# Kernel tuning notes

Hardware: AMD Instinct MI355X
Metric: run time of the kernel (lower is better)

## Reference

```python
import jax, jax.numpy as jnp
import numpy as np

B, F, V, E, T, NTOK, G, D = 8192, 64, 1000, 64, 2, 16, 4, 256
LN_EPS = 1e-5


def setup_inputs() -> dict:
    key = jax.random.key(0)
    ks = jax.random.split(key, 5)
    int_feats = jax.random.randint(ks[0], (B, F), 0, V, dtype=jnp.int64)
    missing_mask = jax.random.randint(ks[1], (B, F), 0, 2, dtype=jnp.int32)
    # deterministic seeded permutation of features split into NTOK equal groups
    perm = np.random.default_rng(1234).permutation(F)
    group_idx = jnp.asarray(perm.reshape(NTOK, G), dtype=jnp.int32)
    emb_tables = jax.random.normal(ks[2], (T, F, V, E), jnp.float32) * 0.02
    missing_emb = jax.random.normal(ks[3], (T, F, E), jnp.float32) * 0.02
    kW, kb = jax.random.split(ks[4])
    W = jax.random.normal(kW, (D, E * T), jnp.float32) * (1.0 / np.sqrt(E * T))
    b = jnp.zeros((D,), jnp.float32)
    ln_gamma = jnp.ones((D,), jnp.float32)
    ln_beta = jnp.zeros((D,), jnp.float32)
    return {"int_feats": int_feats, "missing_mask": missing_mask,
            "group_idx": group_idx, "emb_tables": emb_tables,
            "missing_emb": missing_emb, "W": W, "b": b,
            "ln_gamma": ln_gamma, "ln_beta": ln_beta}


def reference(int_feats, missing_mask, group_idx, emb_tables, missing_emb, W, b, ln_gamma, ln_beta):
    f_idx = jnp.arange(F)[None, :]  # (1, F) broadcast with (B, F) ids
    # per-table feature embedding gather: [T, B, F, E]
    feats = jax.vmap(lambda tbl: tbl[f_idx, int_feats])(emb_tables)
    # additive missing embeddings
    mask = missing_mask.astype(feats.dtype)
    feats = feats + mask[None, :, :, None] * missing_emb[:, None, :, :]
    # token-group mean pooling: [T, B, NTOK, G, E] -> [T, B, NTOK, E]
    pooled = feats[:, :, group_idx, :].mean(axis=3)
    # concat tables along feature dim (table order preserved): [B, NTOK, T*E]
    x = jnp.moveaxis(pooled, 0, 2).reshape(B, NTOK, T * E)
    # Linear -> SiLU -> LayerNorm
    h = jax.nn.silu(x @ W.T + b)
    mu = h.mean(-1, keepdims=True)
    var = ((h - mu) ** 2).mean(-1, keepdims=True)
    return (h - mu) * jax.lax.rsqrt(var + LN_EPS) * ln_gamma + ln_beta
```

## Files before the change

### kernel.cpp

```cpp
#include <hip/hip_runtime.h>
#include <math.h>

#define B_    8192
#define F_    64
#define V_    1000
#define E_    64
#define T_    2
#define NTOK_ 16
#define G_    4
#define D_    256
#define K_    128
#define LN_EPS 1e-5f

#define XSP   136

typedef __attribute__((ext_vector_type(8))) short  frag_ab;
typedef __attribute__((ext_vector_type(4))) float  frag_cd;

static __device__ __forceinline__ unsigned short f2bf(float f) {
    unsigned int u = __float_as_uint(f);
    u += 0x7FFFu + ((u >> 16) & 1u);
    return (unsigned short)(u >> 16);
}

__global__ __launch_bounds__(256) void convert_w_kernel(const float* __restrict__ W,
                                                        unsigned int* __restrict__ Wb_packed) {
    const int i = blockIdx.x * 256 + threadIdx.x;
    if (i < (D_ * K_) / 2) {
        const float2 v = *(const float2*)(W + (size_t)i * 2);
        Wb_packed[i] = (unsigned int)f2bf(v.x) | ((unsigned int)f2bf(v.y) << 16);
    }
}

__global__ __launch_bounds__(256, 8) void fused_tokenizer_kernel(
    const int*   __restrict__ int_feats,
    const int*   __restrict__ missing_mask,
    const int*   __restrict__ group_idx,
    const float* __restrict__ emb_tables,
    const float* __restrict__ missing_emb,
    const unsigned short* __restrict__ Wb,
    const float* __restrict__ bias,
    const float* __restrict__ gamma,
    const float* __restrict__ beta,
    float*       __restrict__ out)
{
    __shared__ unsigned short xs[NTOK_][XSP];
    __shared__ unsigned int   soff[F_];
    __shared__ int            smask[F_];
    __shared__ int            sg[F_];
    __shared__ float          part_s [4][NTOK_];
    __shared__ float          part_ss[4][NTOK_];

    const int tid  = threadIdx.x;
    const int b    = blockIdx.x;
    const int lane = tid & 63;
    const int wave = tid >> 6;
    const int mA   = lane & 15;
    const int q    = lane >> 4;

    if (tid < F_) {
        const int f  = tid;
        const int id = int_feats[b * F_ + f];
        soff[f]  = (unsigned int)((f * V_ + id) * E_);
        smask[f] = missing_mask[b * F_ + f];
        sg[f]    = group_idx[f];
    }
    __syncthreads();

#pragma unroll
    for (int i = 0; i < 2; ++i) {
        const int c  = i * 256 + tid;
        const int n  = c >> 5;
        const int r4 = c & 31;
        const int t  = r4 >> 4;
        const int e  = (r4 & 15) * 4;
        const float* bt = emb_tables + (size_t)t * (F_ * V_ * E_) + e;
        const float* mt = missing_emb + t * (F_ * E_) + e;
        float ax = 0.f, ay = 0.f, az = 0.f, aw = 0.f;
#pragma unroll
        for (int g = 0; g < G_; ++g) {
            const int f = sg[n * G_ + g];
            const float4 v = *(const float4*)(bt + soff[f]);
            float vx = v.x, vy = v.y, vz = v.z, vw = v.w;
            if (smask[f]) {
                const float4 mv = *(const float4*)(mt + f * E_);
                vx += mv.x; vy += mv.y; vz += mv.z; vw += mv.w;
            }
            ax += vx; ay += vy; az += vz; aw += vw;
        }
        unsigned int p0 = (unsigned int)f2bf(0.25f * ax) | ((unsigned int)f2bf(0.25f * ay) << 16);
        unsigned int p1 = (unsigned int)f2bf(0.25f * az) | ((unsigned int)f2bf(0.25f * aw) << 16);
        *(uint2*)(&xs[n][r4 * 4]) = make_uint2(p0, p1);
    }
    __syncthreads();

    frag_ab a[4];
#pragma unroll
    for (int s = 0; s < 4; ++s)
        a[s] = *(const frag_ab*)(&xs[mA][32 * s + 8 * q]);

    float hv[4][4];
    float ps[4]  = {0.f, 0.f, 0.f, 0.f};
    float pss[4] = {0.f, 0.f, 0.f, 0.f};

#pragma unroll
    for (int t = 0; t < 4; ++t) {
        const int nrow = wave * 64 + t * 16 + mA;
        const unsigned short* wp = Wb + (size_t)nrow * K_ + 8 * q;
        frag_cd acc = {0.f, 0.f, 0.f, 0.f};
#pragma unroll
        for (int s = 0; s < 4; ++s) {
            const frag_ab bfr = *(const frag_ab*)(wp + 32 * s);
            acc = __builtin_amdgcn_mfma_f32_16x16x32_bf16(a[s], bfr, acc, 0, 0, 0);
        }
        const float bn = bias[nrow];
#pragma unroll
        for (int reg = 0; reg < 4; ++reg) {
            const float z = acc[reg] + bn;
            const float h = z / (1.f + __expf(-z));
            hv[t][reg] = h;
            ps[reg]  += h;
            pss[reg] += h * h;
        }
    }

#pragma unroll
    for (int off = 1; off < 16; off <<= 1) {
#pragma unroll
        for (int reg = 0; reg < 4; ++reg) {
            ps[reg]  += __shfl_xor(ps[reg],  off, 64);
            pss[reg] += __shfl_xor(pss[reg], off, 64);
        }
    }
    if (mA == 0) {
        *(float4*)(&part_s [wave][q * 4]) = make_float4(ps[0],  ps[1],  ps[2],  ps[3]);
        *(float4*)(&part_ss[wave][q * 4]) = make_float4(pss[0], pss[1], pss[2], pss[3]);
    }
    __syncthreads();

    float4 S0 = *(const float4*)(&part_s [0][q * 4]);
    float4 S1 = *(const float4*)(&part_s [1][q * 4]);
    float4 S2 = *(const float4*)(&part_s [2][q * 4]);
    float4 S3 = *(const float4*)(&part_s [3][q * 4]);
    float4 T0 = *(const float4*)(&part_ss[0][q * 4]);
    float4 T1 = *(const float4*)(&part_ss[1][q * 4]);
    float4 T2 = *(const float4*)(&part_ss[2][q * 4]);
    float4 T3 = *(const float4*)(&part_ss[3][q * 4]);

    float mu[4], rs[4];
    {
        const float s[4]  = {S0.x + S1.x + S2.x + S3.x, S0.y + S1.y + S2.y + S3.y,
                             S0.z + S1.z + S2.z + S3.z, S0.w + S1.w + S2.w + S3.w};
        const float ss[4] = {T0.x + T1.x + T2.x + T3.x, T0.y + T1.y + T2.y + T3.y,
                             T0.z + T1.z + T2.z + T3.z, T0.w + T1.w + T2.w + T3.w};
#pragma unroll
        for (int reg = 0; reg < 4; ++reg) {
            mu[reg] = s[reg] * (1.f / D_);
            const float var = ss[reg] * (1.f / D_) - mu[reg] * mu[reg];
            rs[reg] = rsqrtf(var + LN_EPS);
        }
    }

    const size_t obase = (size_t)b * (NTOK_ * D_);
#pragma unroll
    for (int t = 0; t < 4; ++t) {
        const int col = wave * 64 + t * 16 + mA;
        const float gm = gamma[col];
        const float bb = beta[col];
        float* op = out + obase + col;
#pragma unroll
        for (int reg = 0; reg < 4; ++reg) {
            const int tok = q * 4 + reg;
            op[(size_t)tok * D_] = (hv[t][reg] - mu[reg]) * rs[reg] * gm + bb;
        }
    }
}

extern "C" void kernel_launch(void* const* d_in, const int* in_sizes, int n_in,
                              void* d_out, int out_size, void* d_ws, size_t ws_size,
                              hipStream_t stream) {
    const int*   int_feats    = (const int*)  d_in[0];
    const int*   missing_mask = (const int*)  d_in[1];
    const int*   group_idx    = (const int*)  d_in[2];
    const float* emb_tables   = (const float*)d_in[3];
    const float* missing_emb  = (const float*)d_in[4];
    const float* W            = (const float*)d_in[5];
    const float* bias         = (const float*)d_in[6];
    const float* gamma        = (const float*)d_in[7];
    const float* beta         = (const float*)d_in[8];
    float* out = (float*)d_out;

    unsigned short* Wb = (unsigned short*)d_ws;

    convert_w_kernel<<<(D_ * K_ / 2 + 255) / 256, 256, 0, stream>>>(W, (unsigned int*)Wb);
    fused_tokenizer_kernel<<<B_, 256, 0, stream>>>(
        int_feats, missing_mask, group_idx, emb_tables, missing_emb,
        Wb, bias, gamma, beta, out);
}
```

Baseline: 245.3 us.

## Gather bf16 embedding copies, process four rows per block with prefetch

Each call adds a pre-pass that converts the fp32 embedding and missing tables to bf16 in workspace, halving the bytes read by the random row gather. Each block now handles four batch rows, keeps W fragments plus bias, gamma and beta in registers, and double-buffers the gathers so the next row's loads overlap the current row's MFMA and LayerNorm. The missing flag is packed into the high bit of the offset. The trade-offs are an extra full-table conversion pass on every call, bf16 rounding of the table values before pooling, and higher register pressure. A fall-back fp32 path runs if the workspace is too small.

New measurement: 262.1 us. 6.9% more time.

```diff
diff --git a/kernel.cpp b/kernel.cpp
--- a/kernel.cpp
+++ b/kernel.cpp
@@ -12,167 +12,254 @@
 #define K_    128
 #define LN_EPS 1e-5f
 
+#define R_    4
 #define XSP   136
+
+#define EB_ELEMS (T_*F_*V_*E_)
+#define MB_ELEMS (T_*F_*E_)
+#define WB_ELEMS (D_*K_)
 
 typedef __attribute__((ext_vector_type(8))) short  frag_ab;
 typedef __attribute__((ext_vector_type(4))) float  frag_cd;
+
+template<bool BT> struct GVec;
+template<> struct GVec<true>  { using T = uint2;  };
+template<> struct GVec<false> { using T = float4; };
 
 static __device__ __forceinline__ unsigned short f2bf(float f) {
     unsigned int u = __float_as_uint(f);
     u += 0x7FFFu + ((u >> 16) & 1u);
     return (unsigned short)(u >> 16);
 }
+static __device__ __forceinline__ unsigned int pk2(float a, float b) {
+    return (unsigned int)f2bf(a) | ((unsigned int)f2bf(b) << 16);
+}
+static __device__ __forceinline__ void g2f(uint2 v, float& a, float& b, float& c, float& d) {
+    a = __uint_as_float(v.x << 16);
+    b = __uint_as_float(v.x & 0xFFFF0000u);
+    c = __uint_as_float(v.y << 16);
+    d = __uint_as_float(v.y & 0xFFFF0000u);
+}
+static __device__ __forceinline__ void g2f(float4 v, float& a, float& b, float& c, float& d) {
+    a = v.x; b = v.y; c = v.z; d = v.w;
+}
 
 __global__ __launch_bounds__(256) void convert_w_kernel(const float* __restrict__ W,
                                                         unsigned int* __restrict__ Wb_packed) {
     const int i = blockIdx.x * 256 + threadIdx.x;
-    if (i < (D_ * K_) / 2) {
+    if (i < WB_ELEMS / 2) {
         const float2 v = *(const float2*)(W + (size_t)i * 2);
-        Wb_packed[i] = (unsigned int)f2bf(v.x) | ((unsigned int)f2bf(v.y) << 16);
-    }
-}
-
-__global__ __launch_bounds__(256, 8) void fused_tokenizer_kernel(
+        Wb_packed[i] = pk2(v.x, v.y);
+    }
+}
+
+__global__ __launch_bounds__(256) void convert_tbl_kernel(const float* __restrict__ emb,
+                                                          const float* __restrict__ miss,
+                                                          unsigned int* __restrict__ ebp,
+                                                          unsigned int* __restrict__ mbp) {
+    const int i = blockIdx.x * 256 + threadIdx.x;
+    const int neb = EB_ELEMS / 4;
+    if (i < neb) {
+        const float4 v = *(const float4*)(emb + (size_t)i * 4);
+        ebp[2 * i]     = pk2(v.x, v.y);
+        ebp[2 * i + 1] = pk2(v.z, v.w);
+    } else if (i < neb + MB_ELEMS / 4) {
+        const int j = i - neb;
+        const float4 v = *(const float4*)(miss + (size_t)j * 4);
+        mbp[2 * j]     = pk2(v.x, v.y);
+        mbp[2 * j + 1] = pk2(v.z, v.w);
+    }
+}
+
+template<bool BT, int MINW>
+__global__ __launch_bounds__(256, MINW) void fused_tokenizer_kernel(
     const int*   __restrict__ int_feats,
     const int*   __restrict__ missing_mask,
     const int*   __restrict__ group_idx,
-    const float* __restrict__ emb_tables,
-    const float* __restrict__ missing_emb,
+    const float* __restrict__ embf,
+    const float* __restrict__ missf,
+    const unsigned short* __restrict__ embb,
+    const unsigned short* __restrict__ missb,
     const unsigned short* __restrict__ Wb,
     const float* __restrict__ bias,
     const float* __restrict__ gamma,
     const float* __restrict__ beta,
     float*       __restrict__ out)
 {
-    __shared__ unsigned short xs[NTOK_][XSP];
-    __shared__ unsigned int   soff[F_];
-    __shared__ int            smask[F_];
+    using VT = typename GVec<BT>::T;
+
+    __shared__ unsigned short xs[2][NTOK_][XSP];
+    __shared__ unsigned int   soff[R_][F_];
     __shared__ int            sg[F_];
     __shared__ float          part_s [4][NTOK_];
     __shared__ float          part_ss[4][NTOK_];
 
     const int tid  = threadIdx.x;
-    const int b    = blockIdx.x;
     const int lane = tid & 63;
     const int wave = tid >> 6;
     const int mA   = lane & 15;
     const int q    = lane >> 4;
-
-    if (tid < F_) {
-        const int f  = tid;
-        const int id = int_feats[b * F_ + f];
-        soff[f]  = (unsigned int)((f * V_ + id) * E_);
-        smask[f] = missing_mask[b * F_ + f];
-        sg[f]    = group_idx[f];
-    }
-    __syncthreads();
-
-#pragma unroll
-    for (int i = 0; i < 2; ++i) {
-        const int c  = i * 256 + tid;
-        const int n  = c >> 5;
-        const int r4 = c & 31;
-        const int t  = r4 >> 4;
-        const int e  = (r4 & 15) * 4;
-        const float* bt = emb_tables + (size_t)t * (F_ * V_ * E_) + e;
-        const float* mt = missing_emb + t * (F_ * E_) + e;
-        float ax = 0.f, ay = 0.f, az = 0.f, aw = 0.f;
-#pragma unroll
-        for (int g = 0; g < G_; ++g) {
-            const int f = sg[n * G_ + g];
-            const float4 v = *(const float4*)(bt + soff[f]);
-            float vx = v.x, vy = v.y, vz = v.z, vw = v.w;
-            if (smask[f]) {
-                const float4 mv = *(const float4*)(mt + f * E_);
-                vx += mv.x; vy += mv.y; vz += mv.z; vw += mv.w;
-            }
-            ax += vx; ay += vy; az += vz; aw += vw;
-        }
-        unsigned int p0 = (unsigned int)f2bf(0.25f * ax) | ((unsigned int)f2bf(0.25f * ay) << 16);
-        unsigned int p1 = (unsigned int)f2bf(0.25f * az) | ((unsigned int)f2bf(0.25f * aw) << 16);
-        *(uint2*)(&xs[n][r4 * 4]) = make_uint2(p0, p1);
-    }
-    __syncthreads();
-
-    frag_ab a[4];
-#pragma unroll
-    for (int s = 0; s < 4; ++s)
-        a[s] = *(const frag_ab*)(&xs[mA][32 * s + 8 * q]);
-
-    float hv[4][4];
-    float ps[4]  = {0.f, 0.f, 0.f, 0.f};
-    float pss[4] = {0.f, 0.f, 0.f, 0.f};
-
+    const int r0   = blockIdx.x * R_;
+
+    {
+        const int rr = tid >> 6, f = tid & 63;
+        const int id = int_feats[(r0 + rr) * F_ + f];
+        const unsigned int mk = (unsigned int)missing_mask[(r0 + rr) * F_ + f];
+        soff[rr][f] = (unsigned int)((f * V_ + id) * E_) | (mk << 31);
+        if (tid < F_) sg[tid] = group_idx[tid];
+    }
+
+    frag_ab wfr[4][4];
+    float bias_r[4], gm_r[4], bt_r[4];
 #pragma unroll
     for (int t = 0; t < 4; ++t) {
         const int nrow = wave * 64 + t * 16 + mA;
         const unsigned short* wp = Wb + (size_t)nrow * K_ + 8 * q;
-        frag_cd acc = {0.f, 0.f, 0.f, 0.f};
-#pragma unroll
-        for (int s = 0; s < 4; ++s) {
-            const frag_ab bfr = *(const frag_ab*)(wp + 32 * s);
-            acc = __builtin_amdgcn_mfma_f32_16x16x32_bf16(a[s], bfr, acc, 0, 0, 0);
-        }
-        const float bn = bias[nrow];
-#pragma unroll
-        for (int reg = 0; reg < 4; ++reg) {
-            const float z = acc[reg] + bn;
-            const float h = z / (1.f + __expf(-z));
-            hv[t][reg] = h;
-            ps[reg]  += h;
-            pss[reg] += h * h;
-        }
-    }
-
-#pragma unroll
-    for (int off = 1; off < 16; off <<= 1) {
-#pragma unroll
-        for (int reg = 0; reg < 4; ++reg) {
-            ps[reg]  += __shfl_xor(ps[reg],  off, 64);
-            pss[reg] += __shfl_xor(pss[reg], off, 64);
-        }
-    }
-    if (mA == 0) {
-        *(float4*)(&part_s [wave][q * 4]) = make_float4(ps[0],  ps[1],  ps[2],  ps[3]);
-        *(float4*)(&part_ss[wave][q * 4]) = make_float4(pss[0], pss[1], pss[2], pss[3]);
-    }
+#pragma unroll
+        for (int s = 0; s < 4; ++s) wfr[t][s] = *(const frag_ab*)(wp + 32 * s);
+        bias_r[t] = bias[nrow];
+        gm_r[t]   = gamma[nrow];
+        bt_r[t]   = beta[nrow];
+    }
+
     __syncthreads();
 
-    float4 S0 = *(const float4*)(&part_s [0][q * 4]);
-    float4 S1 = *(const float4*)(&part_s [1][q * 4]);
-    float4 S2 = *(const float4*)(&part_s [2][q * 4]);
-    float4 S3 = *(const float4*)(&part_s [3][q * 4]);
-    float4 T0 = *(const float4*)(&part_ss[0][q * 4]);
-    float4 T1 = *(const float4*)(&part_ss[1][q * 4]);
-    float4 T2 = *(const float4*)(&part_ss[2][q * 4]);
-    float4 T3 = *(const float4*)(&part_ss[3][q * 4]);
-
-    float mu[4], rs[4];
-    {
-        const float s[4]  = {S0.x + S1.x + S2.x + S3.x, S0.y + S1.y + S2.y + S3.y,
-                             S0.z + S1.z + S2.z + S3.z, S0.w + S1.w + S2.w + S3.w};
-        const float ss[4] = {T0.x + T1.x + T2.x + T3.x, T0.y + T1.y + T2.y + T3.y,
-                             T0.z + T1.z + T2.z + T3.z, T0.w + T1.w + T2.w + T3.w};
-#pragma unroll
-        for (int reg = 0; reg < 4; ++reg) {
-            mu[reg] = s[reg] * (1.f / D_);
-            const float var = ss[reg] * (1.f / D_) - mu[reg] * mu[reg];
-            rs[reg] = rsqrtf(var + LN_EPS);
-        }
-    }
-
-    const size_t obase = (size_t)b * (NTOK_ * D_);
-#pragma unroll
-    for (int t = 0; t < 4; ++t) {
-        const int col = wave * 64 + t * 16 + mA;
-        const float gm = gamma[col];
-        const float bb = beta[col];
-        float* op = out + obase + col;
-#pragma unroll
-        for (int reg = 0; reg < 4; ++reg) {
-            const int tok = q * 4 + reg;
-            op[(size_t)tok * D_] = (hv[t][reg] - mu[reg]) * rs[reg] * gm + bb;
-        }
+    VT  mval[2][G_];
+    int fidx[2][G_];
+#pragma unroll
+    for (int i = 0; i < 2; ++i) {
+        const int c = i * 256 + tid, n = c >> 5, r4 = c & 31, tt = r4 >> 4, e = (r4 & 15) * 4;
+#pragma unroll
+        for (int g = 0; g < G_; ++g) {
+            const int f = sg[n * G_ + g];
+            fidx[i][g] = f;
+            const size_t mo = (size_t)(tt * F_ + f) * E_ + e;
+            if constexpr (BT) mval[i][g] = *(const uint2*)(missb + mo);
+            else              mval[i][g] = *(const float4*)(missf + mo);
+        }
+    }
+
+    auto gather_issue = [&](int rr, VT (&gbuf)[2][G_]) {
+#pragma unroll
+        for (int i = 0; i < 2; ++i) {
+            const int c = i * 256 + tid, r4 = c & 31, tt = r4 >> 4, e = (r4 & 15) * 4;
+            const size_t tb = (size_t)tt * (F_ * V_ * E_) + e;
+#pragma unroll
+            for (int g = 0; g < G_; ++g) {
+                const unsigned int so = soff[rr][fidx[i][g]] & 0x7FFFFFFFu;
+                if constexpr (BT) gbuf[i][g] = *(const uint2*)(embb + tb + so);
+                else              gbuf[i][g] = *(const float4*)(embf + tb + so);
+            }
+        }
+    };
+
+    auto pack_write = [&](int rr, unsigned short (&dst)[NTOK_][XSP], VT (&gbuf)[2][G_]) {
+#pragma unroll
+        for (int i = 0; i < 2; ++i) {
+            const int c = i * 256 + tid, n = c >> 5, r4 = c & 31;
+            float ax = 0.f, ay = 0.f, az = 0.f, aw = 0.f;
+#pragma unroll
+            for (int g = 0; g < G_; ++g) {
+                float vx, vy, vz, vw, mx, my, mz, mw;
+                g2f(gbuf[i][g], vx, vy, vz, vw);
+                g2f(mval[i][g], mx, my, mz, mw);
+                const float mf = (soff[rr][fidx[i][g]] >> 31) ? 1.f : 0.f;
+                ax += vx + mf * mx;
+                ay += vy + mf * my;
+                az += vz + mf * mz;
+                aw += vw + mf * mw;
+            }
+            *(uint2*)(&dst[n][r4 * 4]) =
+                make_uint2(pk2(0.25f * ax, 0.25f * ay), pk2(0.25f * az, 0.25f * aw));
+        }
+    };
+
+    VT g0[2][G_], g1[2][G_];
+    gather_issue(0, g0);
+
+#pragma unroll
+    for (int r = 0; r < R_; ++r) {
+        if (r + 1 < R_) gather_issue(r + 1, g1);
+
+        pack_write(r, xs[r & 1], g0);
+        __syncthreads();
+
+        frag_ab a[4];
+#pragma unroll
+        for (int s = 0; s < 4; ++s)
+            a[s] = *(const frag_ab*)(&xs[r & 1][mA][32 * s + 8 * q]);
+
+        float hv[4][4];
+        float ps[4]  = {0.f, 0.f, 0.f, 0.f};
+        float pss[4] = {0.f, 0.f, 0.f, 0.f};
+#pragma unroll
+        for (int t = 0; t < 4; ++t) {
+            frag_cd acc = {0.f, 0.f, 0.f, 0.f};
+#pragma unroll
+            for (int s = 0; s < 4; ++s)
+                acc = __builtin_amdgcn_mfma_f32_16x16x32_bf16(a[s], wfr[t][s], acc, 0, 0, 0);
+#pragma unroll
+            for (int reg = 0; reg < 4; ++reg) {
+                const float z = acc[reg] + bias_r[t];
+                const float h = z / (1.f + __expf(-z));
+                hv[t][reg] = h;
+                ps[reg]  += h;
+                pss[reg] += h * h;
+            }
+        }
+
+#pragma unroll
+        for (int off = 1; off < 16; off <<= 1) {
+#pragma unroll
+            for (int reg = 0; reg < 4; ++reg) {
+                ps[reg]  += __shfl_xor(ps[reg],  off, 64);
+                pss[reg] += __shfl_xor(pss[reg], off, 64);
+            }
+        }
+        if (mA == 0) {
+            *(float4*)(&part_s [wave][q * 4]) = make_float4(ps[0],  ps[1],  ps[2],  ps[3]);
+            *(float4*)(&part_ss[wave][q * 4]) = make_float4(pss[0], pss[1], pss[2], pss[3]);
+        }
+        __syncthreads();
+
+        const float4 S0 = *(const float4*)(&part_s [0][q * 4]);
+        const float4 S1 = *(const float4*)(&part_s [1][q * 4]);
+        const float4 S2 = *(const float4*)(&part_s [2][q * 4]);
+        const float4 S3 = *(const float4*)(&part_s [3][q * 4]);
+        const float4 T0 = *(const float4*)(&part_ss[0][q * 4]);
+        const float4 T1 = *(const float4*)(&part_ss[1][q * 4]);
+        const float4 T2 = *(const float4*)(&part_ss[2][q * 4]);
+        const float4 T3 = *(const float4*)(&part_ss[3][q * 4]);
+
+        float mu[4], rs[4];
+        {
+            const float s[4]  = {S0.x + S1.x + S2.x + S3.x, S0.y + S1.y + S2.y + S3.y,
+                                 S0.z + S1.z + S2.z + S3.z, S0.w + S1.w + S2.w + S3.w};
+            const float ss[4] = {T0.x + T1.x + T2.x + T3.x, T0.y + T1.y + T2.y + T3.y,
+                                 T0.z + T1.z + T2.z + T3.z, T0.w + T1.w + T2.w + T3.w};
+#pragma unroll
+            for (int reg = 0; reg < 4; ++reg) {
+                mu[reg] = s[reg] * (1.f / D_);
+                const float var = ss[reg] * (1.f / D_) - mu[reg] * mu[reg];
+                rs[reg] = rsqrtf(var + LN_EPS);
+            }
+        }
+
+        const size_t obase = (size_t)(r0 + r) * (NTOK_ * D_);
+#pragma unroll
+        for (int t = 0; t < 4; ++t) {
+            const int col = wave * 64 + t * 16 + mA;
+            float* op = out + obase + col;
+#pragma unroll
+            for (int reg = 0; reg < 4; ++reg)
+                op[(size_t)(q * 4 + reg) * D_] =
+                    (hv[t][reg] - mu[reg]) * rs[reg] * gm_r[t] + bt_r[t];
+        }
+
+#pragma unroll
+        for (int i = 0; i < 2; ++i)
+#pragma unroll
+            for (int g = 0; g < G_; ++g) g0[i][g] = g1[i][g];
     }
 }
 
@@ -191,9 +278,21 @@
     float* out = (float*)d_out;
 
     unsigned short* Wb = (unsigned short*)d_ws;
-
-    convert_w_kernel<<<(D_ * K_ / 2 + 255) / 256, 256, 0, stream>>>(W, (unsigned int*)Wb);
-    fused_tokenizer_kernel<<<B_, 256, 0, stream>>>(
-        int_feats, missing_mask, group_idx, emb_tables, missing_emb,
-        Wb, bias, gamma, beta, out);
-}
+    convert_w_kernel<<<(WB_ELEMS / 2 + 255) / 256, 256, 0, stream>>>(W, (unsigned int*)Wb);
+
+    const size_t need = 2ull * (WB_ELEMS + MB_ELEMS + EB_ELEMS);
+    if (ws_size >= need) {
+        unsigned short* Mb = Wb + WB_ELEMS;
+        unsigned short* Eb = Mb + MB_ELEMS;
+        const int nch = (EB_ELEMS + MB_ELEMS) / 4;
+        convert_tbl_kernel<<<(nch + 255) / 256, 256, 0, stream>>>(
+            emb_tables, missing_emb, (unsigned int*)Eb, (unsigned int*)Mb);
+        fused_tokenizer_kernel<true, 3><<<B_ / R_, 256, 0, stream>>>(
+            int_feats, missing_mask, group_idx, nullptr, nullptr, Eb, Mb,
+            Wb, bias, gamma, beta, out);
+    } else {
+        fused_tokenizer_kernel<false, 2><<<B_ / R_, 256, 0, stream>>>(
+            int_feats, missing_mask, group_idx, emb_tables, missing_emb, nullptr, nullptr,
+            Wb, bias, gamma, beta, out);
+    }
+}
```
